# Kernel tuning notes

Hardware: AMD Instinct MI355X
Metric: run time of the kernel (lower is better)

The kernel has to match this reference:

```python
import jax, jax.numpy as jnp
import numpy as np

B, N, DM, S = 128, 1024, 64, 2
D_IN = 1 + 1 + 2 + DM  # x(1) + m(1) + u(2) + h(DM)


def setup_inputs() -> dict:
    key = jax.random.key(0)
    ks = jax.random.split(key, 12)
    return {
        "x": jax.random.normal(ks[0], (B, 1, N), jnp.float32),
        "m": jax.random.uniform(ks[1], (B, 1, N), jnp.float32),
        "u": jax.random.normal(ks[2], (B, 2, N), jnp.float32),
        "h": jax.random.normal(ks[3], (B, DM, N), jnp.float32),
        # stack of support_len row-normalized-ish adjacencies [S, N, N]
        "adj": jax.random.uniform(ks[4], (S, N, N), jnp.float32) / N,
        "W_in": jax.random.normal(ks[5], (DM, D_IN), jnp.float32) * 0.05,
        "b_in": jnp.zeros((DM,), jnp.float32),
        "W_gc": jax.random.normal(ks[6], (DM, S * DM), jnp.float32) * 0.05,
        "b_gc": jnp.zeros((DM,), jnp.float32),
        "W_out": jax.random.normal(ks[7], (DM, 2 * DM), jnp.float32) * 0.05,
        "b_out": jnp.zeros((DM,), jnp.float32),
        "W_read": jax.random.normal(ks[8], (1, 2 * DM), jnp.float32) * 0.05,
        "b_read": jnp.zeros((1,), jnp.float32),
        "prelu_w": jnp.full((1,), 0.25, jnp.float32),
    }


def _conv1x1(x, W, b):
    # Conv1d(kernel_size=1): [b,c,n] x [o,c] -> [b,o,n]
    return jnp.einsum('bcn,oc->bon', x, W) + b[None, :, None]


def reference(x, m, u, h, adj, W_in, b_in, W_gc, b_gc, W_out, b_out, W_read, b_read, prelu_w):
    # concat inputs on channel dim, then 1x1 conv to d_model
    x_in = jnp.concatenate([x, m, u, h], axis=1)            # [b, d_in, n]
    x_in = _conv1x1(x_in, W_in, b_in)                        # [b, dm, n]
    # SpatialConvOrderK (order=1, include_self=False):
    # per-support aggregation einsum('ncvl,wv->ncwl') with l==1
    agg = jnp.einsum('bcv,swv->bscw', x_in, adj)             # [b, S, dm, n]
    b_, s_, c_, n_ = agg.shape
    agg = agg.reshape(b_, s_ * c_, n_)                       # support-major concat
    gc = _conv1x1(agg, W_gc, b_gc)                           # [b, dm, n]
    out = jnp.concatenate([gc, h], axis=1)                   # [b, 2dm, n]
    out = _conv1x1(out, W_out, b_out)
    out = jnp.where(out >= 0, out, prelu_w[0] * out)         # PReLU (1 param)
    out = jnp.concatenate([out, h], axis=1)                  # [b, 2dm, n]
    return _conv1x1(out, W_read, b_read), out
```

## Files before the change

kernel.cpp:

```cpp
#include <hip/hip_runtime.h>
#include <hip/hip_bf16.h>
#include <stdint.h>

#define NB 128
#define NN 1024
#define NDM 64

typedef __bf16 bf16;
typedef __bf16 bf16x8_t __attribute__((ext_vector_type(8)));
typedef __bf16 bf16x4_t __attribute__((ext_vector_type(4)));
typedef float f32x4 __attribute__((ext_vector_type(4)));

__global__ __launch_bounds__(256) void k_prep(
    const float* __restrict__ adj,
    const float* __restrict__ W_in, const float* __restrict__ b_in,
    const float* __restrict__ W_gc, const float* __restrict__ b_gc,
    const float* __restrict__ W_out, const float* __restrict__ b_out,
    const float* __restrict__ W_read,
    bf16* __restrict__ adjb, bf16* __restrict__ WAT, float* __restrict__ WYX,
    float* __restrict__ BIAS, bf16* __restrict__ W1B, bf16* __restrict__ A2B,
    float* __restrict__ HBv) {
  const int bx = blockIdx.x;
  if (bx < 2048) {
    int i = bx * 256 + threadIdx.x;
    float4 v = reinterpret_cast<const float4*>(adj)[i];
    bf16x4_t r;
    r.x = (bf16)v.x; r.y = (bf16)v.y; r.z = (bf16)v.z; r.w = (bf16)v.w;
    reinterpret_cast<bf16x4_t*>(adjb)[i] = r;
    return;
  }
  int i = (bx - 2048) * 256 + threadIdx.x;
  if (i < 8192) {
    int r = i >> 6, cc = i & 63;
    int cq = cc >> 3, j = cc & 7;
    int c = ((cq ^ (r & 7)) << 3) + j;
    int s = r >> 6, o = r & 63;
    float val = 0.f;
    for (int k = 0; k < 64; ++k) val += W_gc[o * 128 + s * 64 + k] * W_in[k * 68 + 4 + c];
    WAT[i] = (bf16)val;
  } else if (i < 8704) {
    int idx = i - 8192;
    int r = idx >> 2, jj = idx & 3;
    int s = r >> 6, o = r & 63;
    float val = 0.f;
    for (int k = 0; k < 64; ++k) val += W_gc[o * 128 + s * 64 + k] * W_in[k * 68 + jj];
    WYX[idx] = val;
  } else if (i < 8832) {
    int r = i - 8704;
    int s = r >> 6, o = r & 63;
    float val = 0.f;
    for (int k = 0; k < 64; ++k) val += W_gc[o * 128 + s * 64 + k] * b_in[k];
    BIAS[r] = val;
  } else if (i < 12928) {
    int j = i - 8832;
    int o = j >> 6, c = j & 63;
    W1B[j] = (bf16)W_out[o * 128 + c];
  } else if (i < 18048) {
    int j = i - 12928;
    int r = j >> 6, c = j & 63;
    float val = 0.f;
    if (r < 64) val = W_out[r * 128 + 64 + c];
    else if (r == 64) val = W_read[64 + c];
    A2B[j] = (bf16)val;
  } else if (i < 18112) {
    int o = i - 18048;
    float val = b_out[o];
    for (int c = 0; c < 64; ++c) val += W_out[o * 128 + c] * b_gc[c];
    HBv[o] = val;
  }
}

__global__ __launch_bounds__(256) void k_build(
    const float* __restrict__ x, const float* __restrict__ m, const float* __restrict__ u,
    const float* __restrict__ h, const bf16* __restrict__ WAT,
    const float* __restrict__ WYX, const float* __restrict__ BIAS,
    bf16* __restrict__ Y, bf16* __restrict__ HT, float* __restrict__ out2) {
  __shared__ __align__(16) float T[64 * 128];
  __shared__ __align__(16) bf16 HTs[128 * 64];
  __shared__ __align__(16) bf16 WAs[128 * 64];
  __shared__ __align__(16) float X4L[128 * 4];
  __shared__ __align__(16) float WYXs[128 * 4];
  __shared__ __align__(16) float biasL[128];
  const int t = threadIdx.x;
  const int vb = blockIdx.x * 128;
  const int b = blockIdx.y;

  for (int i = t; i < 2048; i += 256)
    __builtin_amdgcn_global_load_lds(
        (const uint32_t*)(h + (size_t)(b * 64 + (i >> 5)) * NN + vb + (i & 31) * 4),
        (uint32_t*)&T[i * 4], 16, 0, 0);
  for (int i = t; i < 1024; i += 256)
    __builtin_amdgcn_global_load_lds((const uint32_t*)(WAT + i * 8), (uint32_t*)&WAs[i * 8], 16, 0, 0);
  if (t < 128)
    __builtin_amdgcn_global_load_lds((const uint32_t*)(WYX + t * 4), (uint32_t*)&WYXs[t * 4], 16, 0, 0);
  if (t < 32)
    __builtin_amdgcn_global_load_lds((const uint32_t*)(BIAS + t * 4), (uint32_t*)&biasL[t * 4], 16, 0, 0);
  if (t < 128) {
    float4 x4;
    x4.x = x[(size_t)b * NN + vb + t];
    x4.y = m[(size_t)b * NN + vb + t];
    x4.z = u[(size_t)(b * 2) * NN + vb + t];
    x4.w = u[(size_t)(b * 2 + 1) * NN + vb + t];
    *reinterpret_cast<float4*>(&X4L[t * 4]) = x4;
  }
  __syncthreads();

  {
    const int v = t >> 1, half = t & 1;
#pragma unroll
    for (int cc = 0; cc < 4; ++cc) {
      int cq = half * 4 + cc;
      int cbase = (cq ^ (v & 7)) << 3;
      bf16x8_t pk;
#pragma unroll
      for (int j = 0; j < 8; ++j) pk[j] = (bf16)T[(cbase + j) * 128 + v];
      *reinterpret_cast<bf16x8_t*>(&HTs[v * 64 + cq * 8]) = pk;
      *reinterpret_cast<bf16x8_t*>(&HT[((size_t)(b << 10) + vb + v) * 64 + cq * 8]) = pk;
    }
  }
  for (int i = t; i < 2048; i += 256) {
    int r = i >> 5, ck = i & 31;
    float4 hv = *reinterpret_cast<const float4*>(&T[r * 128 + ck * 4]);
    *reinterpret_cast<float4*>(&out2[(size_t)(b * 128 + 64 + r) * NN + vb + ck * 4]) = hv;
  }
  __syncthreads();

  const int wave = t >> 6, lane = t & 63;
  const int q = lane >> 4, lx = lane & 7, o16 = lane & 15;
  const int offK0 = (q ^ lx) << 3, offK1 = ((q + 4) ^ lx) << 3;

#pragma unroll
  for (int vi = 0; vi < 2; ++vi) {
    const int vt = wave + vi * 4;
    const int vrow = vt * 16 + o16;
    bf16x8_t af0 = *reinterpret_cast<const bf16x8_t*>(&HTs[vrow * 64 + offK0]);
    bf16x8_t af1 = *reinterpret_cast<const bf16x8_t*>(&HTs[vrow * 64 + offK1]);
    float4 x4r[4];
#pragma unroll
    for (int r = 0; r < 4; ++r)
      x4r[r] = *reinterpret_cast<const float4*>(&X4L[(vt * 16 + q * 4 + r) * 4]);
    const int vg = vb + vt * 16 + q * 4;
    for (int nt = 0; nt < 8; ++nt) {
      const int rr = nt * 16 + o16;
      bf16x8_t bf0 = *reinterpret_cast<const bf16x8_t*>(&WAs[rr * 64 + offK0]);
      bf16x8_t bf1 = *reinterpret_cast<const bf16x8_t*>(&WAs[rr * 64 + offK1]);
      float bsv = biasL[rr];
      float4 wy = *reinterpret_cast<const float4*>(&WYXs[rr * 4]);
      f32x4 c0;
#pragma unroll
      for (int r = 0; r < 4; ++r)
        c0[r] = bsv + wy.x * x4r[r].x + wy.y * x4r[r].y + wy.z * x4r[r].z + wy.w * x4r[r].w;
      f32x4 acc = __builtin_amdgcn_mfma_f32_16x16x32_bf16(af0, bf0, c0, 0, 0, 0);
      acc = __builtin_amdgcn_mfma_f32_16x16x32_bf16(af1, bf1, acc, 0, 0, 0);
      const int s = nt >> 2;
      const int o = rr - s * 64;
      bf16x4_t pk;
      pk.x = (bf16)acc[0]; pk.y = (bf16)acc[1]; pk.z = (bf16)acc[2]; pk.w = (bf16)acc[3];
      *reinterpret_cast<bf16x4_t*>(&Y[(size_t)(b * 64 + o) * 2048 + s * 1024 + vg]) = pk;
    }
  }
}

__global__ __launch_bounds__(512, 2) void k_gemm(
    const bf16* __restrict__ Y, const bf16* __restrict__ ADJB,
    const bf16* __restrict__ HT,
    const bf16* __restrict__ W1B, const bf16* __restrict__ A2B,
    const float* __restrict__ HBv, const float* __restrict__ W_read,
    const float* __restrict__ b_read, const float* __restrict__ prelu_w,
    float* __restrict__ out0, float* __restrict__ out2) {
  __shared__ __align__(16) union SMem {
    struct { bf16 As[3][256 * 64]; bf16 Bs[3][128 * 64]; } st;
    struct {
      bf16 gcs[4 * 128 * 72];
      bf16 W1s[64 * 72];
      bf16 A2s[80 * 72];
      float HBs[64];
      float Wrs[64];
    } ep;
  } sm;

  const int t = threadIdx.x;
  const int wave = t >> 6, lane = t & 63;
  const int lin = blockIdx.y * 32 + blockIdx.x;
  const int xcd = lin & 7, rest = lin >> 3;
  const int rowA = (xcd * 4 + (rest >> 3)) * 256;
  const int colB = (rest & 7) * 128;
  const int wm = (wave >> 1) * 64, wn = (wave & 1) * 64;
  const int fr = lane & 15;
  const int q = lane >> 4, lx = lane & 7;
  const int offK0 = (q ^ lx) << 3, offK1 = ((q + 4) ^ lx) << 3;

  f32x4 acc[4][4];
  const f32x4 zero = {0.f, 0.f, 0.f, 0.f};
#pragma unroll
  for (int i = 0; i < 4; ++i)
#pragma unroll
    for (int j = 0; j < 4; ++j) acc[i][j] = zero;

  const bf16* aSrc[4]; const bf16* bSrc[2];
#pragma unroll
  for (int j = 0; j < 4; ++j) {
    const int c = t + 512 * j;
    const int row = c >> 3;
    const int qs = ((c & 7) ^ (row & 7)) << 3;
    aSrc[j] = Y + (size_t)(rowA + row) * 2048 + qs;
  }
#pragma unroll
  for (int j = 0; j < 2; ++j) {
    const int c = t + 512 * j;
    const int row = c >> 3;
    const int qs = ((c & 7) ^ (row & 7)) << 3;
    bSrc[j] = ADJB + (size_t)(colB + row) * 1024 + qs;
  }

  auto stage = [&](int d) {
#pragma unroll
    for (int ja = 0; ja < 4; ++ja) {
      __builtin_amdgcn_global_load_lds((const uint32_t*)aSrc[ja],
                                       (uint32_t*)&sm.st.As[d][(t + 512 * ja) * 8], 16, 0, 0);
      aSrc[ja] += 64;
    }
#pragma unroll
    for (int jb = 0; jb < 2; ++jb) {
      __builtin_amdgcn_global_load_lds((const uint32_t*)bSrc[jb],
                                       (uint32_t*)&sm.st.Bs[d][(t + 512 * jb) * 8], 16, 0, 0);
      bSrc[jb] += 64;
    }
  };

  int rAb[4], rBb[4];
#pragma unroll
  for (int i = 0; i < 4; ++i) {
    rAb[i] = (wm + i * 16 + fr) * 64;
    rBb[i] = (wn + i * 16 + fr) * 64;
  }

  stage(0); stage(1); stage(2);

  int cur = 0;
  for (int kt = 0; kt < 32; ++kt) {
    if (kt < 30)       asm volatile("s_waitcnt vmcnt(12)" ::: "memory");
    else if (kt == 30) asm volatile("s_waitcnt vmcnt(6)" ::: "memory");
    else               asm volatile("s_waitcnt vmcnt(0)" ::: "memory");
    __builtin_amdgcn_s_barrier();
    const bf16* A_ = sm.st.As[cur];
    const bf16* B_ = sm.st.Bs[cur];
    bf16x8_t af0[4], bf0[4], af1[4], bf1[4];
#pragma unroll
    for (int i = 0; i < 4; ++i) af0[i] = *reinterpret_cast<const bf16x8_t*>(&A_[rAb[i] + offK0]);
#pragma unroll
    for (int i = 0; i < 4; ++i) bf0[i] = *reinterpret_cast<const bf16x8_t*>(&B_[rBb[i] + offK0]);
    __builtin_amdgcn_sched_barrier(0);
#pragma unroll
    for (int i = 0; i < 4; ++i) af1[i] = *reinterpret_cast<const bf16x8_t*>(&A_[rAb[i] + offK1]);
#pragma unroll
    for (int i = 0; i < 4; ++i) bf1[i] = *reinterpret_cast<const bf16x8_t*>(&B_[rBb[i] + offK1]);
    asm volatile("s_waitcnt lgkmcnt(8)" ::: "memory");
    __builtin_amdgcn_sched_barrier(0);
    __builtin_amdgcn_s_setprio(1);
#pragma unroll
    for (int i = 0; i < 4; ++i)
#pragma unroll
      for (int j = 0; j < 4; ++j)
        acc[i][j] = __builtin_amdgcn_mfma_f32_16x16x32_bf16(af0[i], bf0[j], acc[i][j], 0, 0, 0);
    __builtin_amdgcn_s_setprio(0);
    asm volatile("s_waitcnt lgkmcnt(0)" ::: "memory");
    __builtin_amdgcn_sched_barrier(0);
    __builtin_amdgcn_s_barrier();
    if (kt < 29) {
      stage(cur);
      if (kt == 12) {
        bSrc[0] += 1024 * 1024 - 1024;
        bSrc[1] += 1024 * 1024 - 1024;
      }
    }
    __builtin_amdgcn_s_setprio(1);
#pragma unroll
    for (int i = 0; i < 4; ++i)
#pragma unroll
      for (int j = 0; j < 4; ++j)
        acc[i][j] = __builtin_amdgcn_mfma_f32_16x16x32_bf16(af1[i], bf1[j], acc[i][j], 0, 0, 0);
    __builtin_amdgcn_s_setprio(0);
    cur = (cur == 2) ? 0 : cur + 1;
  }

  {
    const int r = t >> 3, c8 = t & 7;
    *reinterpret_cast<bf16x8_t*>(&sm.ep.W1s[r * 72 + c8 * 8]) =
        *reinterpret_cast<const bf16x8_t*>(&W1B[t * 8]);
  }
  for (int i = t; i < 640; i += 512) {
    const int r = i >> 3, c8 = i & 7;
    *reinterpret_cast<bf16x8_t*>(&sm.ep.A2s[r * 72 + c8 * 8]) =
        *reinterpret_cast<const bf16x8_t*>(&A2B[i * 8]);
  }
  if (t < 64) { sm.ep.HBs[t] = HBv[t]; sm.ep.Wrs[t] = W_read[t]; }
  const float pw = prelu_w[0];
  const float br = b_read[0];

  {
    const int b2w = wm >> 6;
#pragma unroll
    for (int i = 0; i < 4; ++i) {
      const int cc0 = i * 16 + q * 4;
#pragma unroll
      for (int j = 0; j < 4; ++j) {
        const int wl = wn + j * 16 + fr;
        bf16x4_t r;
        r.x = (bf16)acc[i][j][0]; r.y = (bf16)acc[i][j][1];
        r.z = (bf16)acc[i][j][2]; r.w = (bf16)acc[i][j][3];
        *reinterpret_cast<bf16x4_t*>(&sm.ep.gcs[b2w * 9216 + wl * 72 + cc0]) = r;
      }
    }
  }
  __syncthreads();

  const int b2 = wave >> 1, jh = wave & 1;
  const int b = (rowA >> 6) + b2;

  f32x4 acc2[5][4];
#pragma unroll
  for (int i = 0; i < 5; ++i)
#pragma unroll
    for (int j = 0; j < 4; ++j) {
      if (i < 4) {
        f32x4 c0;
#pragma unroll
        for (int r = 0; r < 4; ++r) c0[r] = sm.ep.HBs[i * 16 + q * 4 + r];
        acc2[i][j] = c0;
      } else {
        acc2[i][j] = zero;
      }
    }

#pragma unroll
  for (int k2 = 0; k2 < 64; k2 += 32) {
    bf16x8_t af2[4], bf2[4];
#pragma unroll
    for (int i = 0; i < 4; ++i)
      af2[i] = *reinterpret_cast<const bf16x8_t*>(&sm.ep.W1s[(i * 16 + fr) * 72 + k2 + q * 8]);
#pragma unroll
    for (int j = 0; j < 4; ++j)
      bf2[j] = *reinterpret_cast<const bf16x8_t*>(&sm.ep.gcs[b2 * 9216 + (jh * 64 + j * 16 + fr) * 72 + k2 + q * 8]);
#pragma unroll
    for (int i = 0; i < 4; ++i)
#pragma unroll
      for (int j = 0; j < 4; ++j)
        acc2[i][j] = __builtin_amdgcn_mfma_f32_16x16x32_bf16(af2[i], bf2[j], acc2[i][j], 0, 0, 0);
  }

#pragma unroll
  for (int k2 = 0; k2 < 64; k2 += 32) {
    const int off = k2 ? offK1 : offK0;
    bf16x8_t bh[4], af3[5];
#pragma unroll
    for (int j = 0; j < 4; ++j) {
      const int w = colB + jh * 64 + j * 16 + fr;
      bh[j] = *reinterpret_cast<const bf16x8_t*>(&HT[((size_t)(b << 10) + w) * 64 + off]);
    }
#pragma unroll
    for (int i = 0; i < 5; ++i)
      af3[i] = *reinterpret_cast<const bf16x8_t*>(&sm.ep.A2s[(i * 16 + fr) * 72 + k2 + q * 8]);
#pragma unroll
    for (int i = 0; i < 5; ++i)
#pragma unroll
      for (int j = 0; j < 4; ++j)
        acc2[i][j] = __builtin_amdgcn_mfma_f32_16x16x32_bf16(af3[i], bh[j], acc2[i][j], 0, 0, 0);
  }

  float rd[4] = {0.f, 0.f, 0.f, 0.f};
#pragma unroll
  for (int i = 0; i < 4; ++i) {
#pragma unroll
    for (int r = 0; r < 4; ++r) {
      const int o = i * 16 + q * 4 + r;
      const float wr = sm.ep.Wrs[o];
#pragma unroll
      for (int j = 0; j < 4; ++j) {
        const int wg = colB + jh * 64 + j * 16 + fr;
        float val = acc2[i][j][r];
        val = val >= 0.f ? val : pw * val;
        out2[(size_t)(b * 128 + o) * 1024 + wg] = val;
        rd[j] += wr * val;
      }
    }
  }
#pragma unroll
  for (int j = 0; j < 4; ++j) {
    rd[j] += __shfl_xor(rd[j], 16, 64);
    rd[j] += __shfl_xor(rd[j], 32, 64);
  }
  if (lane < 16) {
#pragma unroll
    for (int j = 0; j < 4; ++j) {
      const int wg = colB + jh * 64 + j * 16 + lane;
      out0[(size_t)b * 1024 + wg] = rd[j] + acc2[4][j][0] + br;
    }
  }
}

extern "C" void kernel_launch(void* const* d_in, const int* in_sizes, int n_in,
                              void* d_out, int out_size, void* d_ws, size_t ws_size,
                              hipStream_t stream) {
  (void)in_sizes; (void)n_in; (void)out_size; (void)ws_size;
  const float* x       = (const float*)d_in[0];
  const float* m       = (const float*)d_in[1];
  const float* u       = (const float*)d_in[2];
  const float* h       = (const float*)d_in[3];
  const float* adj     = (const float*)d_in[4];
  const float* W_in    = (const float*)d_in[5];
  const float* b_in    = (const float*)d_in[6];
  const float* W_gc    = (const float*)d_in[7];
  const float* b_gc    = (const float*)d_in[8];
  const float* W_out   = (const float*)d_in[9];
  const float* b_out   = (const float*)d_in[10];
  const float* W_read  = (const float*)d_in[11];
  const float* b_read  = (const float*)d_in[12];
  const float* prelu_w = (const float*)d_in[13];

  char* ws = (char*)d_ws;
  bf16*  Y    = (bf16*)(ws);
  bf16*  ADJB = (bf16*)(ws + 33554432);
  bf16*  HT   = (bf16*)(ws + 37748736);
  bf16*  WAT  = (bf16*)(ws + 54525952);
  float* WYX  = (float*)(ws + 54542336);
  float* BIAS = (float*)(ws + 54544384);
  bf16*  W1B  = (bf16*)(ws + 54544896);
  bf16*  A2B  = (bf16*)(ws + 54553088);
  float* HBv  = (float*)(ws + 54563328);

  float* out0 = (float*)d_out;
  float* out2 = out0 + 131072;

  hipLaunchKernelGGL(k_prep,  dim3(2119),     dim3(256), 0, stream,
                     adj, W_in, b_in, W_gc, b_gc, W_out, b_out, W_read,
                     ADJB, WAT, WYX, BIAS, W1B, A2B, HBv);
  hipLaunchKernelGGL(k_build, dim3(8, 128),   dim3(256), 0, stream,
                     x, m, u, h, WAT, WYX, BIAS, Y, HT, out2);
  hipLaunchKernelGGL(k_gemm,  dim3(32, 8),    dim3(512), 0, stream,
                     Y, ADJB, HT, W1B, A2B, HBv, W_read, b_read, prelu_w, out0, out2);
}
```

Before: 182.4 us.

## Load adjacency operand directly to registers with double buffering, skip LDS staging

The B operand (bf16 adjacency tile) is no longer staged through shared memory. Each wave now loads its B fragments straight from global memory into registers, double-buffered across even and odd k-steps. The A-tile pipeline is reworked so the next tile's first-half fragments are prefetched from LDS before the second MFMA batch, with adjusted vmcnt/lgkmcnt waits. This removes LDS traffic and footprint for B, but waves that share the same columns now issue redundant global loads that rely on cache hits.

Result: slower. 220.3 us (+20.8%).

```diff
diff --git a/kernel.cpp b/kernel.cpp
--- a/kernel.cpp
+++ b/kernel.cpp
@@ -169,7 +169,7 @@
     const float* __restrict__ b_read, const float* __restrict__ prelu_w,
     float* __restrict__ out0, float* __restrict__ out2) {
   __shared__ __align__(16) union SMem {
-    struct { bf16 As[3][256 * 64]; bf16 Bs[3][128 * 64]; } st;
+    struct { bf16 As[3][256 * 64]; } st;
     struct {
       bf16 gcs[4 * 128 * 72];
       bf16 W1s[64 * 72];
@@ -197,7 +197,7 @@
 #pragma unroll
     for (int j = 0; j < 4; ++j) acc[i][j] = zero;
 
-  const bf16* aSrc[4]; const bf16* bSrc[2];
+  const bf16* aSrc[4];
 #pragma unroll
   for (int j = 0; j < 4; ++j) {
     const int c = t + 512 * j;
@@ -205,83 +205,88 @@
     const int qs = ((c & 7) ^ (row & 7)) << 3;
     aSrc[j] = Y + (size_t)(rowA + row) * 2048 + qs;
   }
-#pragma unroll
-  for (int j = 0; j < 2; ++j) {
-    const int c = t + 512 * j;
-    const int row = c >> 3;
-    const int qs = ((c & 7) ^ (row & 7)) << 3;
-    bSrc[j] = ADJB + (size_t)(colB + row) * 1024 + qs;
-  }
-
-  auto stage = [&](int d) {
+  auto stageA = [&](int d) {
 #pragma unroll
     for (int ja = 0; ja < 4; ++ja) {
       __builtin_amdgcn_global_load_lds((const uint32_t*)aSrc[ja],
                                        (uint32_t*)&sm.st.As[d][(t + 512 * ja) * 8], 16, 0, 0);
       aSrc[ja] += 64;
     }
-#pragma unroll
-    for (int jb = 0; jb < 2; ++jb) {
-      __builtin_amdgcn_global_load_lds((const uint32_t*)bSrc[jb],
-                                       (uint32_t*)&sm.st.Bs[d][(t + 512 * jb) * 8], 16, 0, 0);
-      bSrc[jb] += 64;
-    }
   };
 
-  int rAb[4], rBb[4];
-#pragma unroll
-  for (int i = 0; i < 4; ++i) {
-    rAb[i] = (wm + i * 16 + fr) * 64;
-    rBb[i] = (wn + i * 16 + fr) * 64;
-  }
-
-  stage(0); stage(1); stage(2);
+  const bf16* pBj[4];
+#pragma unroll
+  for (int j = 0; j < 4; ++j)
+    pBj[j] = ADJB + (size_t)(colB + wn + j * 16 + fr) * 1024 + q * 8;
+  auto loadB = [&](bf16x8_t (&dst)[8], int T) {
+    const size_t ko = ((size_t)(T >> 4) << 20) + (size_t)(T & 15) * 64;
+#pragma unroll
+    for (int j = 0; j < 4; ++j) {
+      dst[j]     = *reinterpret_cast<const bf16x8_t*>(pBj[j] + ko);
+      dst[4 + j] = *reinterpret_cast<const bf16x8_t*>(pBj[j] + ko + 32);
+    }
+  };
+
+  int rAb[4];
+#pragma unroll
+  for (int i = 0; i < 4; ++i) rAb[i] = (wm + i * 16 + fr) * 64;
+
+  bf16x8_t af0[4], af1[4], bfE[8], bfO[8];
+
+  stageA(0); stageA(1);
+  loadB(bfE, 0);
+  asm volatile("s_waitcnt vmcnt(8)" ::: "memory");
+  __builtin_amdgcn_s_barrier();
+  __builtin_amdgcn_sched_barrier(0);
+#pragma unroll
+  for (int i = 0; i < 4; ++i)
+    af0[i] = *reinterpret_cast<const bf16x8_t*>(&sm.st.As[0][rAb[i] + offK0]);
 
   int cur = 0;
-  for (int kt = 0; kt < 32; ++kt) {
-    if (kt < 30)       asm volatile("s_waitcnt vmcnt(12)" ::: "memory");
-    else if (kt == 30) asm volatile("s_waitcnt vmcnt(6)" ::: "memory");
-    else               asm volatile("s_waitcnt vmcnt(0)" ::: "memory");
-    __builtin_amdgcn_s_barrier();
+  auto body = [&](int kt, bf16x8_t (&bfU)[8], bf16x8_t (&bfL)[8]) {
+    const int nxt = (cur == 2) ? 0 : cur + 1;
     const bf16* A_ = sm.st.As[cur];
-    const bf16* B_ = sm.st.Bs[cur];
-    bf16x8_t af0[4], bf0[4], af1[4], bf1[4];
-#pragma unroll
-    for (int i = 0; i < 4; ++i) af0[i] = *reinterpret_cast<const bf16x8_t*>(&A_[rAb[i] + offK0]);
-#pragma unroll
-    for (int i = 0; i < 4; ++i) bf0[i] = *reinterpret_cast<const bf16x8_t*>(&B_[rBb[i] + offK0]);
-    __builtin_amdgcn_sched_barrier(0);
-#pragma unroll
-    for (int i = 0; i < 4; ++i) af1[i] = *reinterpret_cast<const bf16x8_t*>(&A_[rAb[i] + offK1]);
-#pragma unroll
-    for (int i = 0; i < 4; ++i) bf1[i] = *reinterpret_cast<const bf16x8_t*>(&B_[rBb[i] + offK1]);
-    asm volatile("s_waitcnt lgkmcnt(8)" ::: "memory");
+#pragma unroll
+    for (int i = 0; i < 4; ++i)
+      af1[i] = *reinterpret_cast<const bf16x8_t*>(&A_[rAb[i] + offK1]);
+    asm volatile("s_waitcnt lgkmcnt(4)" ::: "memory");
     __builtin_amdgcn_sched_barrier(0);
     __builtin_amdgcn_s_setprio(1);
 #pragma unroll
     for (int i = 0; i < 4; ++i)
 #pragma unroll
       for (int j = 0; j < 4; ++j)
-        acc[i][j] = __builtin_amdgcn_mfma_f32_16x16x32_bf16(af0[i], bf0[j], acc[i][j], 0, 0, 0);
+        acc[i][j] = __builtin_amdgcn_mfma_f32_16x16x32_bf16(af0[i], bfU[j], acc[i][j], 0, 0, 0);
     __builtin_amdgcn_s_setprio(0);
+    if (kt < 31) loadB(bfL, kt + 1);
     asm volatile("s_waitcnt lgkmcnt(0)" ::: "memory");
     __builtin_amdgcn_sched_barrier(0);
+    asm volatile("s_waitcnt vmcnt(8)" ::: "memory");
     __builtin_amdgcn_s_barrier();
-    if (kt < 29) {
-      stage(cur);
-      if (kt == 12) {
-        bSrc[0] += 1024 * 1024 - 1024;
-        bSrc[1] += 1024 * 1024 - 1024;
-      }
+    __builtin_amdgcn_sched_barrier(0);
+    if (kt < 30) {
+      const int stg = (nxt == 2) ? 0 : nxt + 1;
+      stageA(stg);
+    }
+    if (kt < 31) {
+      const bf16* An = sm.st.As[nxt];
+#pragma unroll
+      for (int i = 0; i < 4; ++i)
+        af0[i] = *reinterpret_cast<const bf16x8_t*>(&An[rAb[i] + offK0]);
     }
     __builtin_amdgcn_s_setprio(1);
 #pragma unroll
     for (int i = 0; i < 4; ++i)
 #pragma unroll
       for (int j = 0; j < 4; ++j)
-        acc[i][j] = __builtin_amdgcn_mfma_f32_16x16x32_bf16(af1[i], bf1[j], acc[i][j], 0, 0, 0);
+        acc[i][j] = __builtin_amdgcn_mfma_f32_16x16x32_bf16(af1[i], bfU[4 + j], acc[i][j], 0, 0, 0);
     __builtin_amdgcn_s_setprio(0);
-    cur = (cur == 2) ? 0 : cur + 1;
+    cur = nxt;
+  };
+
+  for (int mi = 0; mi < 16; ++mi) {
+    body(2 * mi,     bfE, bfO);
+    body(2 * mi + 1, bfO, bfE);
   }
 
   {
```
